# Kernel tuning notes

Measured on AMD Instinct MI355X. Metric: run time of the kernel, lower is better.

Reference implementation:

```python
import jax, jax.numpy as jnp
import numpy as np

N_NODES = 50000


def gcn_conv(x, src, dst, norm, W, b, n):
    # PyG GCNConv: out = A_hat @ (x W) + b, with A_hat = D^-1/2 (A+I) D^-1/2
    h = x @ W                                   # [N, out]
    msgs = norm[:, None] * h[src]               # [E+N, out]
    out = jax.ops.segment_sum(msgs, dst, num_segments=n)
    return out + b


def _norm_and_loops(edge_index, n):
    # add self loops
    loops = jnp.arange(n, dtype=edge_index.dtype)
    src = jnp.concatenate([edge_index[0], loops])
    dst = jnp.concatenate([edge_index[1], loops])
    ones = jnp.ones(src.shape[0], dtype=jnp.float32)
    deg = jax.ops.segment_sum(ones, dst, num_segments=n)
    dinv = jnp.where(deg > 0, jax.lax.rsqrt(jnp.maximum(deg, 1e-12)), 0.0)
    norm = dinv[src] * dinv[dst]
    return src, dst, norm


def setup_inputs() -> dict:
    key = jax.random.key(0)
    k1, k2, k3, k4, k5, k6 = jax.random.split(key, 6)
    F_in, H, C = 1433, 128, 7
    x = jax.random.normal(k1, (N_NODES, F_in), dtype=jnp.float32)
    edge_index = jax.random.randint(k2, (2, 1600000), 0, N_NODES, dtype=jnp.int64)
    W1 = jax.random.normal(k3, (F_in, H), dtype=jnp.float32) / np.sqrt(F_in)
    b1 = jnp.zeros((H,), dtype=jnp.float32)
    W2 = jax.random.normal(k4, (H, C), dtype=jnp.float32) / np.sqrt(H)
    b2 = jnp.zeros((C,), dtype=jnp.float32)
    return {"x": x, "edge_index": edge_index, "W1": W1, "b1": b1, "W2": W2, "b2": b2}


def reference(x, edge_index, W1, b1, W2, b2):
    n = x.shape[0]
    src, dst, norm = _norm_and_loops(edge_index, n)
    h = gcn_conv(x, src, dst, norm, W1, b1, n)
    h = jax.nn.relu(h)
    # dropout p=0.5 is identity in eval mode
    out = gcn_conv(h, src, dst, norm, W2, b2, n)
    return out
```

## Files before the change

### kernel.cpp

```cpp
#include <hip/hip_runtime.h>
#include <hip/hip_bf16.h>

typedef __attribute__((ext_vector_type(8))) short short8_t;
typedef __attribute__((ext_vector_type(4))) float f32x4;
typedef float f32x4u __attribute__((ext_vector_type(4), aligned(4)));
typedef int i32x4 __attribute__((ext_vector_type(4)));

#define NNODES 50000
#define FIN 1433
#define HID 128
#define NCLS 7
#define KT1 45
#define BK 32
#define BM 128
#define CAP 96
#define GSTR 1040

static __device__ __forceinline__ unsigned short f2bf(float f) {
    union { float f; unsigned int u; } v; v.f = f;
    unsigned int u = v.u;
    u += 0x7FFFu + ((u >> 16) & 1u);
    return (unsigned short)(u >> 16);
}
static __device__ __forceinline__ float u2f(unsigned int u) {
    union { unsigned int u; float f; } v; v.u = u; return v.f;
}

__global__ void prep_w1(const float* __restrict__ W1, unsigned short* __restrict__ W1s) {
    int tid = blockIdx.x * 512 + threadIdx.x;
    if (tid >= KT1 * 512) return;
    int kt = tid >> 9, seg = tid & 511;
    int c = seg & 127, g = seg >> 7;
    int kb = kt * BK + g * 8;
    unsigned int w[4];
    #pragma unroll
    for (int p = 0; p < 4; ++p) {
        int k0 = kb + p * 2, k1 = kb + p * 2 + 1;
        unsigned short lo = (k0 < FIN) ? f2bf(W1[(size_t)k0 * HID + c]) : (unsigned short)0;
        unsigned short hi = (k1 < FIN) ? f2bf(W1[(size_t)k1 * HID + c]) : (unsigned short)0;
        w[p] = (unsigned int)lo | ((unsigned int)hi << 16);
    }
    uint4* dstp = (uint4*)(W1s + (size_t)tid * 8);
    uint4 val; val.x = w[0]; val.y = w[1]; val.z = w[2]; val.w = w[3];
    *dstp = val;
}

__global__ __launch_bounds__(512) void gemm_fill(const float* __restrict__ x,
                                                 const unsigned short* __restrict__ W1s,
                                                 unsigned short* __restrict__ h, int M,
                                                 const int* __restrict__ src,
                                                 const int* __restrict__ dst, int E,
                                                 int* __restrict__ cnt,
                                                 int* __restrict__ csr_f,
                                                 int* __restrict__ ovf_cnt,
                                                 int2* __restrict__ ovf, int gb) {
    __shared__ unsigned short As[2][4160];
    __shared__ unsigned short Bs[3][4096];

    if (blockIdx.x >= gb) {
        int bid = blockIdx.x - gb;
        int i = (bid * 512 + (int)threadIdx.x) * 8;
        if (i + 7 < E) {
            i32x4 d0 = __builtin_nontemporal_load((const i32x4*)(dst + i));
            i32x4 d1 = __builtin_nontemporal_load((const i32x4*)(dst + i + 4));
            i32x4 s0 = __builtin_nontemporal_load((const i32x4*)(src + i));
            i32x4 s1 = __builtin_nontemporal_load((const i32x4*)(src + i + 4));
            int dd[8] = {d0.x, d0.y, d0.z, d0.w, d1.x, d1.y, d1.z, d1.w};
            int ss[8] = {s0.x, s0.y, s0.z, s0.w, s1.x, s1.y, s1.z, s1.w};
            #pragma unroll
            for (int e = 0; e < 8; ++e) {
                int pos = atomicAdd(&cnt[dd[e]], 1);
                if (pos < CAP) __builtin_nontemporal_store(ss[e], &csr_f[dd[e] * CAP + pos]);
                else { int op = atomicAdd(ovf_cnt, 1); ovf[op] = make_int2(dd[e], ss[e]); }
            }
        } else if (i < E) {
            for (int e = i; e < E; ++e) {
                int d = dst[e], s = src[e];
                int pos = atomicAdd(&cnt[d], 1);
                if (pos < CAP) csr_f[d * CAP + pos] = s;
                else { int op = atomicAdd(ovf_cnt, 1); ovf[op] = make_int2(d, s); }
            }
        }
        return;
    }

    const int t = threadIdx.x;
    const int wave = t >> 6, lane = t & 63;
    const int wm = wave >> 1, wn = wave & 1;
    const int r = lane & 15, u = lane >> 4;
    const int rowBase = blockIdx.x * BM;
    f32x4 acc[2][4] = {};

    float4 areg[2];

    auto issueA = [&](int kt) {
        int k0 = kt * BK;
        #pragma unroll
        for (int i = 0; i < 2; ++i) {
            int quad = i * 512 + t;
            int row = quad >> 3, kq = quad & 7;
            int gr = min(rowBase + row, M - 1);
            int gk = k0 + kq * 4;
            f32x4u v = *(const f32x4u*)(x + (size_t)gr * FIN + gk);
            areg[i].x = v.x; areg[i].y = v.y; areg[i].z = v.z; areg[i].w = v.w;
        }
    };
    auto issueA_tail = [&]() {
        #pragma unroll
        for (int i = 0; i < 2; ++i) {
            int quad = i * 512 + t;
            int row = quad >> 3, kq = quad & 7;
            int gr = min(rowBase + row, M - 1);
            int gk = 1408 + kq * 4;
            const float* p = x + (size_t)gr * FIN;
            areg[i].x = (gk + 0 < FIN) ? p[gk + 0] : 0.f;
            areg[i].y = (gk + 1 < FIN) ? p[gk + 1] : 0.f;
            areg[i].z = (gk + 2 < FIN) ? p[gk + 2] : 0.f;
            areg[i].w = (gk + 3 < FIN) ? p[gk + 3] : 0.f;
        }
    };
    auto issueB = [&](int kt, int buf) {
        const unsigned short* gp = W1s + ((size_t)kt * 512 + t) * 8;
        unsigned short* lp = &Bs[buf][(wave * 64) * 8];
        __builtin_amdgcn_global_load_lds(
            (const __attribute__((address_space(1))) unsigned int*)gp,
            (__attribute__((address_space(3))) unsigned int*)lp, 16, 0, 0);
    };
    auto writeA = [&](int buf) {
        #pragma unroll
        for (int i = 0; i < 2; ++i) {
            int quad = i * 512 + t;
            int row = quad >> 3, kq = quad & 7;
            __hip_bfloat162 lo2 = __float22bfloat162_rn(make_float2(areg[i].x, areg[i].y));
            __hip_bfloat162 hi2 = __float22bfloat162_rn(make_float2(areg[i].z, areg[i].w));
            unsigned int ulo, uhi;
            __builtin_memcpy(&ulo, &lo2, 4);
            __builtin_memcpy(&uhi, &hi2, 4);
            unsigned long long pk = ((unsigned long long)uhi << 32) | (unsigned long long)ulo;
            int g = kq >> 1, half = kq & 1;
            int us = ((g ^ (row & 3)) * GSTR) + row * 8 + half * 4;
            *(unsigned long long*)(&As[buf][us]) = pk;
        }
    };
    auto compute = [&](int kt) {
        const int abuf = kt & 1, bbuf = kt % 3;
        short8_t af[2], bfr[4];
        #pragma unroll
        for (int mi = 0; mi < 2; ++mi) {
            int row = wm * 32 + mi * 16 + r;
            int us = ((u ^ (row & 3)) * GSTR) + row * 8;
            af[mi] = *(const short8_t*)(&As[abuf][us]);
        }
        #pragma unroll
        for (int ni = 0; ni < 4; ++ni) {
            int c = wn * 64 + ni * 16 + r;
            bfr[ni] = *(const short8_t*)(&Bs[bbuf][u * 1024 + c * 8]);
        }
        #pragma unroll
        for (int mi = 0; mi < 2; ++mi)
            #pragma unroll
            for (int ni = 0; ni < 4; ++ni)
                acc[mi][ni] = __builtin_amdgcn_mfma_f32_16x16x32_bf16(af[mi], bfr[ni], acc[mi][ni], 0, 0, 0);
    };

    issueA(0); issueB(0, 0);
    writeA(0);
    issueA(1); issueB(1, 1);
    __syncthreads();

    for (int kt = 0; kt < KT1 - 3; ++kt) {
        compute(kt);
        writeA((kt + 1) & 1);
        issueA(kt + 2);
        issueB(kt + 2, (kt + 2) % 3);
        __syncthreads();
    }
    {
        compute(KT1 - 3);
        writeA((KT1 - 2) & 1);
        __syncthreads();
    }
    issueA_tail();
    issueB(KT1 - 1, (KT1 - 1) % 3);
    writeA((KT1 - 1) & 1);
    __syncthreads();
    compute(KT1 - 2);
    compute(KT1 - 1);

    #pragma unroll
    for (int mi = 0; mi < 2; ++mi) {
        #pragma unroll
        for (int reg = 0; reg < 4; ++reg) {
            int grow = rowBase + wm * 32 + mi * 16 + u * 4 + reg;
            if (grow < M) {
                #pragma unroll
                for (int ni = 0; ni < 4; ++ni) {
                    int gcol = wn * 64 + ni * 16 + r;
                    h[(size_t)grow * HID + gcol] = f2bf(acc[mi][ni][reg]);
                }
            }
        }
    }
}

__global__ void self_dinv(int* __restrict__ cnt, int* __restrict__ csr_f,
                          float* __restrict__ dinv,
                          int* __restrict__ ovf_cnt, int2* __restrict__ ovf, int n) {
    int i = blockIdx.x * 256 + threadIdx.x;
    if (i >= n) return;
    int c = cnt[i];
    if (c < CAP) csr_f[i * CAP + c] = i;
    else { int op = atomicAdd(ovf_cnt, 1); ovf[op] = make_int2(i, i); }
    cnt[i] = c + 1;
    dinv[i] = rsqrtf((float)(c + 1));
}

__global__ __launch_bounds__(256) void agg1(const unsigned short* __restrict__ h,
                                            const int* __restrict__ cnt,
                                            const int* __restrict__ csr_f,
                                            const float* __restrict__ dinv,
                                            const float* __restrict__ b1,
                                            const float* __restrict__ W2,
                                            const int* __restrict__ ovf_cnt,
                                            const int2* __restrict__ ovf,
                                            float* __restrict__ h2s, int n) {
    __shared__ float W2s[HID * NCLS];
    for (int i = threadIdx.x; i < HID * NCLS; i += 256) W2s[i] = W2[i];
    __syncthreads();
    int wave = threadIdx.x >> 6, lane = threadIdx.x & 63;
    int v = blockIdx.x * 4 + wave;
    if (v >= n) return;
    const int fr = lane & 15, g = lane >> 4;
    int total = cnt[v];
    int inrow = min(total, CAP);
    const int base = v * CAP;
    float acc[8] = {};
    #pragma unroll 4
    for (int j = g; j < inrow; j += 4) {
        int s = csr_f[base + j];
        float ds = dinv[s];
        uint4 q = *(const uint4*)(h + (size_t)s * HID + fr * 8);
        unsigned int w[4] = {q.x, q.y, q.z, q.w};
        #pragma unroll
        for (int p = 0; p < 4; ++p) {
            acc[p * 2 + 0] += ds * u2f(w[p] << 16);
            acc[p * 2 + 1] += ds * u2f(w[p] & 0xffff0000u);
        }
    }
    if (__builtin_expect(total > CAP, 0) && g == 0) {
        int on = *ovf_cnt;
        for (int k = 0; k < on; ++k) {
            int2 pr = ovf[k];
            if (pr.x == v) {
                int s = pr.y;
                float ds = dinv[s];
                uint4 q = *(const uint4*)(h + (size_t)s * HID + fr * 8);
                unsigned int w[4] = {q.x, q.y, q.z, q.w};
                #pragma unroll
                for (int p = 0; p < 4; ++p) {
                    acc[p * 2 + 0] += ds * u2f(w[p] << 16);
                    acc[p * 2 + 1] += ds * u2f(w[p] & 0xffff0000u);
                }
            }
        }
    }
    #pragma unroll
    for (int e = 0; e < 8; ++e) {
        acc[e] += __shfl_xor(acc[e], 16, 64);
        acc[e] += __shfl_xor(acc[e], 32, 64);
    }
    float dv = dinv[v];
    float p[NCLS];
    #pragma unroll
    for (int c = 0; c < NCLS; ++c) p[c] = 0.f;
    #pragma unroll
    for (int e = 0; e < 8; ++e) {
        int f = fr * 8 + e;
        float val = fmaxf(dv * acc[e] + b1[f], 0.f);
        #pragma unroll
        for (int c = 0; c < NCLS; ++c) p[c] += val * W2s[f * NCLS + c];
    }
    #pragma unroll
    for (int off = 8; off >= 1; off >>= 1)
        #pragma unroll
        for (int c = 0; c < NCLS; ++c)
            p[c] += __shfl_xor(p[c], off, 64);
    if (lane == 0) {
        #pragma unroll
        for (int c = 0; c < NCLS; ++c) h2s[(size_t)v * 8 + c] = dv * p[c];
        h2s[(size_t)v * 8 + 7] = 0.f;
    }
}

__global__ __launch_bounds__(256) void agg2(const float* __restrict__ h2s,
                                            const int* __restrict__ cnt,
                                            const int* __restrict__ csr_f,
                                            const float* __restrict__ dinv,
                                            const float* __restrict__ b2,
                                            const int* __restrict__ ovf_cnt,
                                            const int2* __restrict__ ovf,
                                            float* __restrict__ out, int n) {
    int wave = threadIdx.x >> 6, lane = threadIdx.x & 63;
    int half = lane >> 5;
    int c = lane & 7, g = (lane >> 3) & 3;
    int v = blockIdx.x * 8 + wave * 2 + half;
    if (v >= n) return;
    int total = cnt[v];
    int inrow = min(total, CAP);
    const int base = v * CAP;
    float acc = 0.f;
    #pragma unroll 4
    for (int j = g; j < inrow; j += 4) {
        int s = csr_f[base + j];
        acc += h2s[(size_t)s * 8 + c];
    }
    if (__builtin_expect(total > CAP, 0) && g == 0) {
        int on = *ovf_cnt;
        for (int k = 0; k < on; ++k) {
            int2 pr = ovf[k];
            if (pr.x == v) acc += h2s[(size_t)pr.y * 8 + c];
        }
    }
    acc += __shfl_xor(acc, 8, 64);
    acc += __shfl_xor(acc, 16, 64);
    if (g == 0 && c < NCLS) out[(size_t)v * NCLS + c] = dinv[v] * acc + b2[c];
}

extern "C" void kernel_launch(void* const* d_in, const int* in_sizes, int n_in,
                              void* d_out, int out_size, void* d_ws, size_t ws_size,
                              hipStream_t stream) {
    const float* x  = (const float*)d_in[0];
    const int*   ei = (const int*)d_in[1];
    const float* W1 = (const float*)d_in[2];
    const float* b1 = (const float*)d_in[3];
    const float* W2 = (const float*)d_in[4];
    const float* b2 = (const float*)d_in[5];
    float* out = (float*)d_out;

    const int N = NNODES;
    const int E = in_sizes[1] / 2;
    const int* src = ei;
    const int* dst = ei + E;
    const int GB = (N + BM - 1) / BM;
    const int FB = (E + 4095) / 4096;

    char* ws = (char*)d_ws;
    size_t off = 0;
    auto alloc = [&](size_t bytes) {
        void* p = ws + off;
        off += (bytes + 255) & ~(size_t)255;
        return p;
    };
    int*   cnt     = (int*)alloc((size_t)N * 4);
    int*   ovf_cnt = (int*)alloc(4);
    float* dinv    = (float*)alloc((size_t)N * 4);
    int*   csr_f   = (int*)alloc((size_t)N * CAP * 4);
    int2*  ovf     = (int2*)alloc((size_t)4096 * 8);
    unsigned short* W1s = (unsigned short*)alloc((size_t)KT1 * 512 * 8 * 2);
    unsigned short* h   = (unsigned short*)alloc((size_t)N * HID * 2);
    float* h2s     = (float*)alloc((size_t)N * 8 * 4);

    (void)hipMemsetAsync(cnt, 0, ((char*)ovf_cnt - (char*)cnt) + 256, stream);
    prep_w1<<<(KT1 * 512 + 511) / 512, 512, 0, stream>>>(W1, W1s);
    gemm_fill<<<GB + FB, 512, 0, stream>>>(x, W1s, h, N, src, dst, E,
                                           cnt, csr_f, ovf_cnt, ovf, GB);
    self_dinv<<<(N + 255) / 256, 256, 0, stream>>>(cnt, csr_f, dinv, ovf_cnt, ovf, N);
    agg1<<<(N + 3) / 4, 256, 0, stream>>>(h, cnt, csr_f, dinv, b1, W2, ovf_cnt, ovf, h2s, N);
    agg2<<<(N + 7) / 8, 256, 0, stream>>>(h2s, cnt, csr_f, dinv, b2, ovf_cnt, ovf, out, N);
}
```

Measured before the change: 244.7 us.

## Halve GEMM row tile to 64 and double edges per fill block

The row tile of the fused GEMM+CSR-fill kernel shrinks from 128 to 64 rows, so each wave handles one 16-row MFMA slice instead of two, and the LDS A buffers and swizzle stride shrink to match. This doubles the number of GEMM blocks, which gives better load spread across CUs and lower per-block register and LDS use. The cost is that each W1 tile now feeds half as many rows, so W1 is fetched from L2 twice as often. The edge-fill blocks now each process two 4096-edge chunks, and their nontemporal loads and stores become plain loads and stores.

```diff
diff --git a/kernel.cpp b/kernel.cpp
--- a/kernel.cpp
+++ b/kernel.cpp
@@ -4,7 +4,6 @@
 typedef __attribute__((ext_vector_type(8))) short short8_t;
 typedef __attribute__((ext_vector_type(4))) float f32x4;
 typedef float f32x4u __attribute__((ext_vector_type(4), aligned(4)));
-typedef int i32x4 __attribute__((ext_vector_type(4)));
 
 #define NNODES 50000
 #define FIN 1433
@@ -12,9 +11,9 @@
 #define NCLS 7
 #define KT1 45
 #define BK 32
-#define BM 128
+#define BM 64
 #define CAP 96
-#define GSTR 1040
+#define GSTR 520
 
 static __device__ __forceinline__ unsigned short f2bf(float f) {
     union { float f; unsigned int u; } v; v.f = f;
@@ -54,31 +53,34 @@
                                                  int* __restrict__ csr_f,
                                                  int* __restrict__ ovf_cnt,
                                                  int2* __restrict__ ovf, int gb) {
-    __shared__ unsigned short As[2][4160];
+    __shared__ unsigned short As[2][2080];
     __shared__ unsigned short Bs[3][4096];
 
     if (blockIdx.x >= gb) {
         int bid = blockIdx.x - gb;
-        int i = (bid * 512 + (int)threadIdx.x) * 8;
-        if (i + 7 < E) {
-            i32x4 d0 = __builtin_nontemporal_load((const i32x4*)(dst + i));
-            i32x4 d1 = __builtin_nontemporal_load((const i32x4*)(dst + i + 4));
-            i32x4 s0 = __builtin_nontemporal_load((const i32x4*)(src + i));
-            i32x4 s1 = __builtin_nontemporal_load((const i32x4*)(src + i + 4));
-            int dd[8] = {d0.x, d0.y, d0.z, d0.w, d1.x, d1.y, d1.z, d1.w};
-            int ss[8] = {s0.x, s0.y, s0.z, s0.w, s1.x, s1.y, s1.z, s1.w};
-            #pragma unroll
-            for (int e = 0; e < 8; ++e) {
-                int pos = atomicAdd(&cnt[dd[e]], 1);
-                if (pos < CAP) __builtin_nontemporal_store(ss[e], &csr_f[dd[e] * CAP + pos]);
-                else { int op = atomicAdd(ovf_cnt, 1); ovf[op] = make_int2(dd[e], ss[e]); }
-            }
-        } else if (i < E) {
-            for (int e = i; e < E; ++e) {
-                int d = dst[e], s = src[e];
-                int pos = atomicAdd(&cnt[d], 1);
-                if (pos < CAP) csr_f[d * CAP + pos] = s;
-                else { int op = atomicAdd(ovf_cnt, 1); ovf[op] = make_int2(d, s); }
+        #pragma unroll
+        for (int half = 0; half < 2; ++half) {
+            int i = (bid * 1024 + half * 512 + (int)threadIdx.x) * 8;
+            if (i + 7 < E) {
+                int4 d0 = *(const int4*)(dst + i);
+                int4 d1 = *(const int4*)(dst + i + 4);
+                int4 s0 = *(const int4*)(src + i);
+                int4 s1 = *(const int4*)(src + i + 4);
+                int dd[8] = {d0.x, d0.y, d0.z, d0.w, d1.x, d1.y, d1.z, d1.w};
+                int ss[8] = {s0.x, s0.y, s0.z, s0.w, s1.x, s1.y, s1.z, s1.w};
+                #pragma unroll
+                for (int e = 0; e < 8; ++e) {
+                    int pos = atomicAdd(&cnt[dd[e]], 1);
+                    if (pos < CAP) csr_f[dd[e] * CAP + pos] = ss[e];
+                    else { int op = atomicAdd(ovf_cnt, 1); ovf[op] = make_int2(dd[e], ss[e]); }
+                }
+            } else if (i < E) {
+                for (int e = i; e < E; ++e) {
+                    int d = dst[e], s = src[e];
+                    int pos = atomicAdd(&cnt[d], 1);
+                    if (pos < CAP) csr_f[d * CAP + pos] = s;
+                    else { int op = atomicAdd(ovf_cnt, 1); ovf[op] = make_int2(d, s); }
+                }
             }
         }
         return;
@@ -89,35 +91,27 @@
     const int wm = wave >> 1, wn = wave & 1;
     const int r = lane & 15, u = lane >> 4;
     const int rowBase = blockIdx.x * BM;
-    f32x4 acc[2][4] = {};
-
-    float4 areg[2];
+    f32x4 acc[4] = {};
+
+    float4 areg;
 
     auto issueA = [&](int kt) {
         int k0 = kt * BK;
-        #pragma unroll
-        for (int i = 0; i < 2; ++i) {
-            int quad = i * 512 + t;
-            int row = quad >> 3, kq = quad & 7;
-            int gr = min(rowBase + row, M - 1);
-            int gk = k0 + kq * 4;
-            f32x4u v = *(const f32x4u*)(x + (size_t)gr * FIN + gk);
-            areg[i].x = v.x; areg[i].y = v.y; areg[i].z = v.z; areg[i].w = v.w;
-        }
+        int row = t >> 3, kq = t & 7;
+        int gr = min(rowBase + row, M - 1);
+        int gk = k0 + kq * 4;
+        f32x4u v = *(const f32x4u*)(x + (size_t)gr * FIN + gk);
+        areg.x = v.x; areg.y = v.y; areg.z = v.z; areg.w = v.w;
     };
     auto issueA_tail = [&]() {
-        #pragma unroll
-        for (int i = 0; i < 2; ++i) {
-            int quad = i * 512 + t;
-            int row = quad >> 3, kq = quad & 7;
-            int gr = min(rowBase + row, M - 1);
-            int gk = 1408 + kq * 4;
-            const float* p = x + (size_t)gr * FIN;
-            areg[i].x = (gk + 0 < FIN) ? p[gk + 0] : 0.f;
-            areg[i].y = (gk + 1 < FIN) ? p[gk + 1] : 0.f;
-            areg[i].z = (gk + 2 < FIN) ? p[gk + 2] : 0.f;
-            areg[i].w = (gk + 3 < FIN) ? p[gk + 3] : 0.f;
-        }
+        int row = t >> 3, kq = t & 7;
+        int gr = min(rowBase + row, M - 1);
+        int gk = 1408 + kq * 4;
+        const float* p = x + (size_t)gr * FIN;
+        areg.x = (gk + 0 < FIN) ? p[gk + 0] : 0.f;
+        areg.y = (gk + 1 < FIN) ? p[gk + 1] : 0.f;
+        areg.z = (gk + 2 < FIN) ? p[gk + 2] : 0.f;
+        areg.w = (gk + 3 < FIN) ? p[gk + 3] : 0.f;
     };
     auto issueB = [&](int kt, int buf) {
         const unsigned short* gp = W1s + ((size_t)kt * 512 + t) * 8;
@@ -127,29 +121,24 @@
             (__attribute__((address_space(3))) unsigned int*)lp, 16, 0, 0);
     };
     auto writeA = [&](int buf) {
-        #pragma unroll
-        for (int i = 0; i < 2; ++i) {
-            int quad = i * 512 + t;
-            int row = quad >> 3, kq = quad & 7;
-            __hip_bfloat162 lo2 = __float22bfloat162_rn(make_float2(areg[i].x, areg[i].y));
-            __hip_bfloat162 hi2 = __float22bfloat162_rn(make_float2(areg[i].z, areg[i].w));
-            unsigned int ulo, uhi;
-            __builtin_memcpy(&ulo, &lo2, 4);
-            __builtin_memcpy(&uhi, &hi2, 4);
-            unsigned long long pk = ((unsigned long long)uhi << 32) | (unsigned long long)ulo;
-            int g = kq >> 1, half = kq & 1;
-            int us = ((g ^ (row & 3)) * GSTR) + row * 8 + half * 4;
-            *(unsigned long long*)(&As[buf][us]) = pk;
-        }
+        int row = t >> 3, kq = t & 7;
+        __hip_bfloat162 lo2 = __float22bfloat162_rn(make_float2(areg.x, areg.y));
+        __hip_bfloat162 hi2 = __float22bfloat162_rn(make_float2(areg.z, areg.w));
+        unsigned int ulo, uhi;
+        __builtin_memcpy(&ulo, &lo2, 4);
+        __builtin_memcpy(&uhi, &hi2, 4);
+        unsigned long long pk = ((unsigned long long)uhi << 32) | (unsigned long long)ulo;
+        int g = kq >> 1, half = kq & 1;
+        int us = ((g ^ (row & 3)) * GSTR) + row * 8 + half * 4;
+        *(unsigned long long*)(&As[buf][us]) = pk;
     };
     auto compute = [&](int kt) {
         const int abuf = kt & 1, bbuf = kt % 3;
-        short8_t af[2], bfr[4];
-        #pragma unroll
-        for (int mi = 0; mi < 2; ++mi) {
-            int row = wm * 32 + mi * 16 + r;
+        short8_t af, bfr[4];
+        {
+            int row = wm * 16 + r;
             int us = ((u ^ (row & 3)) * GSTR) + row * 8;
-            af[mi] = *(const short8_t*)(&As[abuf][us]);
+            af = *(const short8_t*)(&As[abuf][us]);
         }
         #pragma unroll
         for (int ni = 0; ni < 4; ++ni) {
@@ -157,10 +146,8 @@
             bfr[ni] = *(const short8_t*)(&Bs[bbuf][u * 1024 + c * 8]);
         }
         #pragma unroll
-        for (int mi = 0; mi < 2; ++mi)
-            #pragma unroll
-            for (int ni = 0; ni < 4; ++ni)
-                acc[mi][ni] = __builtin_amdgcn_mfma_f32_16x16x32_bf16(af[mi], bfr[ni], acc[mi][ni], 0, 0, 0);
+        for (int ni = 0; ni < 4; ++ni)
+            acc[ni] = __builtin_amdgcn_mfma_f32_16x16x32_bf16(af, bfr[ni], acc[ni], 0, 0, 0);
     };
 
     issueA(0); issueB(0, 0);
@@ -188,16 +175,13 @@
     compute(KT1 - 1);
 
     #pragma unroll
-    for (int mi = 0; mi < 2; ++mi) {
-        #pragma unroll
-        for (int reg = 0; reg < 4; ++reg) {
-            int grow = rowBase + wm * 32 + mi * 16 + u * 4 + reg;
-            if (grow < M) {
-                #pragma unroll
-                for (int ni = 0; ni < 4; ++ni) {
-                    int gcol = wn * 64 + ni * 16 + r;
-                    h[(size_t)grow * HID + gcol] = f2bf(acc[mi][ni][reg]);
-                }
+    for (int reg = 0; reg < 4; ++reg) {
+        int grow = rowBase + wm * 16 + u * 4 + reg;
+        if (grow < M) {
+            #pragma unroll
+            for (int ni = 0; ni < 4; ++ni) {
+                int gcol = wn * 64 + ni * 16 + r;
+                h[(size_t)grow * HID + gcol] = f2bf(acc[ni][reg]);
             }
         }
     }
@@ -342,7 +326,7 @@
     const int* src = ei;
     const int* dst = ei + E;
     const int GB = (N + BM - 1) / BM;
-    const int FB = (E + 4095) / 4096;
+    const int FB = (E + 8191) / 8192;
 
     char* ws = (char*)d_ws;
     size_t off = 0;
```

New measurement: 238.7 us. 2.5% less time.
